# Kernel tuning notes

Hardware: AMD Instinct MI355X
Metric: run time of the kernel (lower is better)

## Reference

```python
import jax, jax.numpy as jnp
import numpy as np

N_NODES = 60000
N_EDGES = 960000
IN_C = 128
HID = 4 * IN_C       # 512
D_CAT = 8 * IN_C     # 1024
D_FC = 16 * IN_C     # 2048
D_L1 = 32 * IN_C     # 4096
OUT_C = 64
BN_EPS = 1e-5
LEAKY_SLOPE = 0.01


def setup_inputs() -> dict:
    key = jax.random.key(0)
    ks = jax.random.split(key, 32)
    d = {}
    d['x'] = jax.random.normal(ks[0], (N_NODES, IN_C), dtype=jnp.float32)
    d['edge_index'] = jax.random.randint(ks[1], (2, N_EDGES), 0, N_NODES, dtype=jnp.int64)

    def lin(k, fan_in, fan_out):
        k1, k2 = jax.random.split(k)
        bound = 1.0 / np.sqrt(fan_in)
        w = jax.random.uniform(k1, (fan_in, fan_out), jnp.float32, -bound, bound)
        b = jax.random.uniform(k2, (fan_out,), jnp.float32, -bound, bound)
        return w, b

    # GIN conv A MLP: Linear(IN_C,HID) -> BN(HID) -> ReLU -> Linear(HID,HID) -> ReLU
    d['w1a'], d['b1a'] = lin(ks[2], IN_C, HID)
    d['gamma_a'] = jnp.ones((HID,), jnp.float32)
    d['beta_a'] = jnp.zeros((HID,), jnp.float32)
    d['mean_a'] = jax.random.normal(ks[3], (HID,), jnp.float32) * 0.1
    d['var_a'] = jax.random.uniform(ks[4], (HID,), jnp.float32, 0.5, 1.5)
    d['w2a'], d['b2a'] = lin(ks[5], HID, HID)
    # GIN conv B MLP
    d['w1b'], d['b1b'] = lin(ks[6], IN_C, HID)
    d['gamma_b'] = jnp.ones((HID,), jnp.float32)
    d['beta_b'] = jnp.zeros((HID,), jnp.float32)
    d['mean_b'] = jax.random.normal(ks[7], (HID,), jnp.float32) * 0.1
    d['var_b'] = jax.random.uniform(ks[8], (HID,), jnp.float32, 0.5, 1.5)
    d['w2b'], d['b2b'] = lin(ks[9], HID, HID)
    # dense head
    d['fc_w'], d['fc_b'] = lin(ks[10], D_CAT, D_FC)
    d['l1_w'], d['l1_b'] = lin(ks[11], D_FC, D_L1)
    d['l2_w'], d['l2_b'] = lin(ks[12], D_L1, D_FC)
    d['out_w'], d['out_b'] = lin(ks[13], D_FC, OUT_C)
    return d


def _gin_conv(x, edge_index, w1, b1, gamma, beta, mean, var, w2, b2):
    # GINConv, eps=0: h_i = MLP(x_i + sum_{j->i} x_j)
    src, dst = edge_index[0], edge_index[1]
    agg = jax.ops.segment_sum(x[src], dst, num_segments=x.shape[0])
    h = x + agg
    h = h @ w1 + b1
    # BatchNorm1d in eval mode (running stats)
    h = (h - mean) * jax.lax.rsqrt(var + BN_EPS) * gamma + beta
    h = jax.nn.relu(h)
    h = jax.nn.relu(h @ w2 + b2)
    return h


def reference(x, edge_index, w1a, b1a, gamma_a, beta_a, mean_a, var_a, w2a, b2a,
              w1b, b1b, gamma_b, beta_b, mean_b, var_b, w2b, b2b,
              fc_w, fc_b, l1_w, l1_b, l2_w, l2_b, out_w, out_b):
    x1 = _gin_conv(x, edge_index, w1a, b1a, gamma_a, beta_a, mean_a, var_a, w2a, b2a)
    x2 = _gin_conv(x, edge_index, w1b, b1b, gamma_b, beta_b, mean_b, var_b, w2b, b2b)
    h = jnp.concatenate([x1, x2], axis=1)               # [N, 8*in]
    h = jax.nn.leaky_relu(h @ fc_w + fc_b, LEAKY_SLOPE)  # dropout is identity in eval
    h = h @ l1_w + l1_b
    h = h @ l2_w + l2_b
    h = jax.nn.sigmoid(h @ out_w + out_b)
    return h
```

## Files before the change

### kernel.cpp

```cpp
#include <hip/hip_runtime.h>


#define NN 60000
#define NE 960000
#define C_IN 128
#define HID 512
#define DCAT 1024
#define DFC 2048
#define DL1 4096
#define OUTC 64

typedef __bf16 bf16x8 __attribute__((ext_vector_type(8)));
typedef float floatx4 __attribute__((ext_vector_type(4)));

__device__ __forceinline__ unsigned short f2b(float f) {
  unsigned int u = __float_as_uint(f);
  unsigned int r = (u + 0x7fffu + ((u >> 16) & 1u)) >> 16;
  return (unsigned short)r;
}

#define GLOAD_LDS16(g, l)                                                     \
  __builtin_amdgcn_global_load_lds(                                           \
      (__attribute__((address_space(1))) void*)(g),                           \
      (__attribute__((address_space(3))) void*)(l), 16, 0, 0)

__global__ void k_bnparams(const float* __restrict__ g,
                           const float* __restrict__ be,
                           const float* __restrict__ mn,
                           const float* __restrict__ vr,
                           const float* __restrict__ b1,
                           float* __restrict__ scale, float* __restrict__ shift) {
  int i = blockIdx.x * 256 + threadIdx.x;
  if (i < HID) {
    float s = g[i] * rsqrtf(vr[i] + 1e-5f);
    scale[i] = s;
    shift[i] = (b1[i] - mn[i]) * s + be[i];
  }
}

__global__ void k_transpose(const float* __restrict__ in,
                            unsigned short* __restrict__ out, int K, int N) {
  __shared__ float t[32][33];
  int n0 = blockIdx.x * 32, k0 = blockIdx.y * 32;
  int tx = threadIdx.x & 31, ty = threadIdx.x >> 5;
#pragma unroll
  for (int i = 0; i < 32; i += 8)
    t[ty + i][tx] = in[(size_t)(k0 + ty + i) * N + n0 + tx];
  __syncthreads();
#pragma unroll
  for (int i = 0; i < 32; i += 8)
    out[(size_t)(n0 + ty + i) * K + k0 + tx] = f2b(t[tx][ty + i]);
}

__global__ void k_deg(const int* __restrict__ dst, int* __restrict__ deg) {
  int e = blockIdx.x * 256 + threadIdx.x;
  if (e < NE) atomicAdd(&deg[dst[e]], 1);
}

__global__ void k_scan1(const int* __restrict__ deg, int* __restrict__ offs,
                        int* __restrict__ bsum) {
  __shared__ int t[256];
  int i = blockIdx.x * 256 + threadIdx.x;
  int v = (i < NN) ? deg[i] : 0;
  t[threadIdx.x] = v;
  __syncthreads();
#pragma unroll
  for (int d = 1; d < 256; d <<= 1) {
    int add = (threadIdx.x >= d) ? t[threadIdx.x - d] : 0;
    __syncthreads();
    t[threadIdx.x] += add;
    __syncthreads();
  }
  if (i < NN) offs[i] = t[threadIdx.x] - v;
  if (threadIdx.x == 255) bsum[blockIdx.x] = t[255];
}

__global__ void k_scan2(int* __restrict__ bsum, int nb) {
  __shared__ int t[256];
  int v = (threadIdx.x < nb) ? bsum[threadIdx.x] : 0;
  t[threadIdx.x] = v;
  __syncthreads();
#pragma unroll
  for (int d = 1; d < 256; d <<= 1) {
    int add = (threadIdx.x >= d) ? t[threadIdx.x - d] : 0;
    __syncthreads();
    t[threadIdx.x] += add;
    __syncthreads();
  }
  if (threadIdx.x < nb) bsum[threadIdx.x] = t[threadIdx.x] - v;
}

__global__ void k_scan3(int* __restrict__ offs, const int* __restrict__ bsum,
                        int* __restrict__ cursor) {
  int i = blockIdx.x * 256 + threadIdx.x;
  if (i < NN) {
    int o = offs[i] + bsum[blockIdx.x];
    offs[i] = o;
    cursor[i] = o;
  }
  if (i == 0) offs[NN] = NE;
}

__global__ void k_bucket(const int* __restrict__ src, const int* __restrict__ dst,
                         int* __restrict__ cursor, int* __restrict__ esrc) {
  int e = blockIdx.x * 256 + threadIdx.x;
  if (e < NE) {
    int slot = atomicAdd(&cursor[dst[e]], 1);
    esrc[slot] = src[e];
  }
}

__global__ void k_agg(const float2* __restrict__ x2, const int* __restrict__ offs,
                      const int* __restrict__ esrc, unsigned int* __restrict__ h0u) {
  int node = blockIdx.x * 4 + (threadIdx.x >> 6);
  if (node >= NN) return;
  int lane = threadIdx.x & 63;
  int beg = offs[node], end = offs[node + 1];
  float2 acc = x2[(size_t)node * 64 + lane];
  for (int j = beg; j < end; j++) {
    int s = esrc[j];
    float2 v = x2[(size_t)s * 64 + lane];
    acc.x += v.x;
    acc.y += v.y;
  }
  h0u[(size_t)node * 64 + lane] =
      (unsigned)f2b(acc.x) | ((unsigned)f2b(acc.y) << 16);
}

template <int EPI>
__device__ __forceinline__ void gemm_epilogue(
    floatx4 (&acc)[8][4], unsigned short* C, const float* bias,
    const float* scale, const float* shift, int M, int N, int ldc, int m0,
    int n0, int w, int quad, int r16) {
#pragma unroll
  for (int j = 0; j < 4; j++) {
    int gn = n0 + w * 64 + j * 16 + r16;
    int cn = gn < N ? gn : 0;
    float p0, p1 = 0.f;
    if constexpr (EPI == 2) {
      p0 = scale[cn];
      p1 = shift[cn];
    } else {
      p0 = bias[cn];
    }
#pragma unroll
    for (int i = 0; i < 8; i++) {
#pragma unroll
      for (int t = 0; t < 4; t++) {
        int gm = m0 + i * 16 + quad * 4 + t;
        if (gm < M && gn < N) {
          float v = acc[i][j][t];
          if constexpr (EPI == 0) {
            v += p0;
            C[(size_t)gm * ldc + gn] = f2b(v);
          } else if constexpr (EPI == 1) {
            v += p0; v = v > 0.f ? v : 0.f;
            C[(size_t)gm * ldc + gn] = f2b(v);
          } else if constexpr (EPI == 2) {
            v = v * p0 + p1; v = v > 0.f ? v : 0.f;
            C[(size_t)gm * ldc + gn] = f2b(v);
          } else if constexpr (EPI == 3) {
            v += p0; v = v > 0.f ? v : 0.01f * v;
            C[(size_t)gm * ldc + gn] = f2b(v);
          } else {
            v += p0;
            v = 1.f / (1.f + __expf(-v));
            ((float*)C)[(size_t)gm * ldc + gn] = v;
          }
        }
      }
    }
  }
}

__device__ __forceinline__ void gemm_swizzle(int M, int N, int& m0, int& n0) {
  const int mt_total = (M + 127) >> 7, nt_total = (N + 255) >> 8;
  int mt, nt;
  if ((nt_total & 7) == 0) {
    const int ntpx = nt_total >> 3;
    const int x = blockIdx.x & 7;
    const int s = blockIdx.x >> 3;
    nt = x * ntpx + (s % ntpx);
    mt = s / ntpx;
  } else {
    const int GM = 8;
    const int full = (mt_total / GM) * GM;
    const int boundary = full * nt_total;
    int id = blockIdx.x;
    if (id < boundary) {
      int per_group = GM * nt_total;
      int g = id / per_group, r = id % per_group;
      mt = g * GM + r % GM;
      nt = r / GM;
    } else {
      int r = id - boundary, gm = mt_total - full;
      mt = full + r % gm;
      nt = r / gm;
    }
  }
  m0 = mt << 7;
  n0 = nt << 8;
}

__device__ __forceinline__ void gemm_swizzle256(int M, int N, int& m0, int& n0) {
  const int mt_total = (M + 255) >> 8, nt_total = N >> 8;
  int mt, nt;
  if ((nt_total & 7) == 0) {
    const int ntpx = nt_total >> 3;
    const int x = blockIdx.x & 7;
    const int s = blockIdx.x >> 3;
    nt = x * ntpx + (s % ntpx);
    mt = s / ntpx;
  } else {
    const int GM = 8;
    const int full = (mt_total / GM) * GM;
    const int boundary = full * nt_total;
    int id = blockIdx.x;
    if (id < boundary) {
      int per_group = GM * nt_total;
      int g = id / per_group, r = id % per_group;
      mt = g * GM + r % GM;
      nt = r / GM;
    } else {
      int r = id - boundary, gm = mt_total - full;
      mt = full + r % gm;
      nt = r / gm;
    }
  }
  m0 = mt << 8;
  n0 = nt << 8;
}

template <int EPI>
__global__ __launch_bounds__(256, 2) void k_gemm_g(
    const unsigned short* __restrict__ A, const unsigned short* __restrict__ Bt,
    unsigned short* __restrict__ C, const float* __restrict__ bias,
    const float* __restrict__ scale, const float* __restrict__ shift,
    int M, int N, int K, int lda, int ldc) {
  __shared__ __align__(16) unsigned short lsA[4][4][128][8];

  const int tid = threadIdx.x;
  const int w = tid >> 6;
  const int lane = tid & 63;
  const int quad = lane >> 4;
  const int r16 = lane & 15;

  int m0, n0;
  gemm_swizzle(M, N, m0, n0);

  const int ra0 = min(m0 + lane, M - 1);
  const int ra1 = min(m0 + 64 + lane, M - 1);
  const unsigned short* pA0 = A + (size_t)ra0 * lda + w * 8;
  const unsigned short* pA1 = A + (size_t)ra1 * lda + w * 8;
  const unsigned short* pB[4];
#pragma unroll
  for (int j = 0; j < 4; j++) {
    int rb = min(n0 + w * 64 + j * 16 + r16, N - 1);
    pB[j] = Bt + (size_t)rb * K + quad * 8;
  }

  floatx4 acc[8][4];
#pragma unroll
  for (int i = 0; i < 8; i++)
#pragma unroll
    for (int j = 0; j < 4; j++) acc[i][j] = (floatx4){0.f, 0.f, 0.f, 0.f};

  const int niter = K >> 5;

#define ISSUE_A(st)                                                           \
  do {                                                                        \
    GLOAD_LDS16(pA0, &lsA[st][w][0][0]);                                      \
    GLOAD_LDS16(pA1, &lsA[st][w][64][0]);                                     \
    pA0 += 32; pA1 += 32;                                                     \
  } while (0)

  ISSUE_A(0);
  if (niter > 1) ISSUE_A(1);
  if (niter > 2) ISSUE_A(2);
  bf16x8 bcur[4], bnxt[4];
#pragma unroll
  for (int j = 0; j < 4; j++) {
    bcur[j] = *(const bf16x8*)pB[j];
    pB[j] += 32;
  }

  int st = 0;
  for (int t = 0; t < niter; t++) {
    if (t + 2 < niter) {
      asm volatile("s_waitcnt vmcnt(8)\n\ts_barrier" ::: "memory");
    } else if (t + 1 < niter) {
      asm volatile("s_waitcnt vmcnt(6)\n\ts_barrier" ::: "memory");
    } else {
      asm volatile("s_waitcnt vmcnt(4)\n\ts_barrier" ::: "memory");
    }
    if (t + 3 < niter) {
      int s3 = st + 3;
      if (s3 >= 4) s3 -= 4;
      ISSUE_A(s3);
    }
    if (t + 1 < niter) {
#pragma unroll
      for (int j = 0; j < 4; j++) {
        bnxt[j] = *(const bf16x8*)pB[j];
        pB[j] += 32;
      }
    }

    bf16x8 af[8];
#pragma unroll
    for (int i = 0; i < 8; i++)
      af[i] = *(const bf16x8*)&lsA[st][quad][i * 16 + r16][0];
#pragma unroll
    for (int j = 0; j < 4; j++)
#pragma unroll
      for (int i = 0; i < 8; i++)
        acc[i][j] = __builtin_amdgcn_mfma_f32_16x16x32_bf16(af[i], bcur[j],
                                                            acc[i][j], 0, 0, 0);
#pragma unroll
    for (int j = 0; j < 4; j++) bcur[j] = bnxt[j];
    st = (st + 1) & 3;
  }
#undef ISSUE_A

  gemm_epilogue<EPI>(acc, C, bias, scale, shift, M, N, ldc, m0, n0, w, quad, r16);
}

template <int EPI>
__global__ __launch_bounds__(512, 2) void k_gemm8(
    const unsigned short* __restrict__ A, const unsigned short* __restrict__ Bt,
    unsigned short* __restrict__ C, const float* __restrict__ bias,
    const float* __restrict__ scale, const float* __restrict__ shift,
    int M, int N, int K, int lda, int ldc) {
  __shared__ __align__(16) unsigned short smem[2][2][256][64];

  const int tid = threadIdx.x;
  const int w = tid >> 6;
  const int lane = tid & 63;
  const int wm = w >> 2;
  const int wn = w & 3;
  const int quad = lane >> 4;
  const int r16 = lane & 15;

  int m0, n0;
  gemm_swizzle256(M, N, m0, n0);

  const int w8l = w * 8 + (lane >> 3);
  const int csrc = (lane & 7) ^ ((lane >> 3) & 7);
  unsigned offA[2][2], offB[2][2];
#pragma unroll
  for (int h = 0; h < 2; h++)
#pragma unroll
    for (int q = 0; q < 2; q++) {
      int ra = m0 + h * 128 + q * 64 + w8l;
      ra = ra < M ? ra : (M - 1);
      offA[h][q] = (unsigned)ra * (unsigned)(lda * 2) + (unsigned)(csrc * 16);
      int rb = n0 + h * 128 + q * 64 + w8l;
      offB[h][q] = (unsigned)rb * (unsigned)(K * 2) + (unsigned)(csrc * 16);
    }
  const char* Ac = (const char*)A;
  const char* Bc = (const char*)Bt;
  char* smc = (char*)smem;
  const unsigned wdst = (unsigned)(w * 1024);

#define STG_A(T_, h_)                                                          \
  do {                                                                         \
    unsigned kb_ = (unsigned)(T_) * 128u;                                      \
    unsigned db_ = (unsigned)(((T_) & 1) << 16) + (unsigned)((h_) * 16384) + wdst; \
    GLOAD_LDS16(Ac + offA[h_][0] + kb_, smc + db_);                            \
    GLOAD_LDS16(Ac + offA[h_][1] + kb_, smc + db_ + 8192u);                    \
  } while (0)
#define STG_B(T_, h_)                                                          \
  do {                                                                         \
    unsigned kb_ = (unsigned)(T_) * 128u;                                      \
    unsigned db_ = (unsigned)(((T_) & 1) << 16) + 32768u +                     \
                   (unsigned)((h_) * 16384) + wdst;                            \
    GLOAD_LDS16(Bc + offB[h_][0] + kb_, smc + db_);                            \
    GLOAD_LDS16(Bc + offB[h_][1] + kb_, smc + db_ + 8192u);                    \
  } while (0)

  const int swz = r16 & 7;
  const unsigned cK0 = (unsigned)(((quad) ^ swz) * 16);
  const unsigned cK1 = (unsigned)(((4 + quad) ^ swz) * 16);
  const unsigned rdA = (unsigned)((wm * 128 + r16) * 128);
  const unsigned rdB = 32768u + (unsigned)((wn * 64 + r16) * 128);

#define RD_A(bo_, i_, c_) (*(const bf16x8*)(smc + (bo_) + rdA + (unsigned)((i_)*2048) + (c_)))
#define RD_B(bo_, j_, c_) (*(const bf16x8*)(smc + (bo_) + rdB + (unsigned)((j_)*2048) + (c_)))

  floatx4 acc[8][4];
#pragma unroll
  for (int i = 0; i < 8; i++)
#pragma unroll
    for (int j = 0; j < 4; j++) acc[i][j] = (floatx4){0.f, 0.f, 0.f, 0.f};

  const int NT = K >> 6;

  STG_B(0, 0); STG_B(0, 1); STG_A(0, 0); STG_A(0, 1);
  if (NT > 1) {
    STG_B(1, 0); STG_B(1, 1); STG_A(1, 0); STG_A(1, 1);
    asm volatile("s_waitcnt vmcnt(8)\n\ts_barrier" ::: "memory");
  } else {
    asm volatile("s_waitcnt vmcnt(0)\n\ts_barrier" ::: "memory");
  }

  bf16x8 aF[4][2], bL[2][2], bH[2][2];

  for (int T = 0; T < NT; T++) {
    const unsigned bo = (unsigned)((T & 1) << 16);
#pragma unroll
    for (int i = 0; i < 4; i++) { aF[i][0] = RD_A(bo, i, cK0); aF[i][1] = RD_A(bo, i, cK1); }
#pragma unroll
    for (int j = 0; j < 2; j++) { bL[j][0] = RD_B(bo, j, cK0); bL[j][1] = RD_B(bo, j, cK1); }
    asm volatile("s_barrier" ::: "memory");
    asm volatile("s_waitcnt lgkmcnt(0)" ::: "memory");
    __builtin_amdgcn_s_setprio(1);
#pragma unroll
    for (int j = 0; j < 2; j++)
#pragma unroll
      for (int i = 0; i < 4; i++) {
        acc[i][j] = __builtin_amdgcn_mfma_f32_16x16x32_bf16(aF[i][0], bL[j][0], acc[i][j], 0, 0, 0);
        acc[i][j] = __builtin_amdgcn_mfma_f32_16x16x32_bf16(aF[i][1], bL[j][1], acc[i][j], 0, 0, 0);
      }
    __builtin_amdgcn_s_setprio(0);
    asm volatile("s_barrier" ::: "memory");
#pragma unroll
    for (int j = 0; j < 2; j++) { bH[j][0] = RD_B(bo, j + 2, cK0); bH[j][1] = RD_B(bo, j + 2, cK1); }
    asm volatile("s_barrier" ::: "memory");
    asm volatile("s_waitcnt lgkmcnt(0)" ::: "memory");
    __builtin_amdgcn_s_setprio(1);
#pragma unroll
    for (int j = 0; j < 2; j++)
#pragma unroll
      for (int i = 0; i < 4; i++) {
        acc[i][j + 2] = __builtin_amdgcn_mfma_f32_16x16x32_bf16(aF[i][0], bH[j][0], acc[i][j + 2], 0, 0, 0);
        acc[i][j + 2] = __builtin_amdgcn_mfma_f32_16x16x32_bf16(aF[i][1], bH[j][1], acc[i][j + 2], 0, 0, 0);
      }
    __builtin_amdgcn_s_setprio(0);
    asm volatile("s_barrier" ::: "memory");
#pragma unroll
    for (int i = 0; i < 4; i++) { aF[i][0] = RD_A(bo, i + 4, cK0); aF[i][1] = RD_A(bo, i + 4, cK1); }
    if (T + 2 < NT) { STG_B(T + 2, 0); STG_B(T + 2, 1); }
    asm volatile("s_barrier" ::: "memory");
    asm volatile("s_waitcnt lgkmcnt(0)" ::: "memory");
    __builtin_amdgcn_s_setprio(1);
#pragma unroll
    for (int j = 0; j < 2; j++)
#pragma unroll
      for (int i = 0; i < 4; i++) {
        acc[i + 4][j + 2] = __builtin_amdgcn_mfma_f32_16x16x32_bf16(aF[i][0], bH[j][0], acc[i + 4][j + 2], 0, 0, 0);
        acc[i + 4][j + 2] = __builtin_amdgcn_mfma_f32_16x16x32_bf16(aF[i][1], bH[j][1], acc[i + 4][j + 2], 0, 0, 0);
      }
    __builtin_amdgcn_s_setprio(0);
    asm volatile("s_barrier" ::: "memory");
    if (T + 2 < NT) { STG_A(T + 2, 0); STG_A(T + 2, 1); }
    asm volatile("s_barrier" ::: "memory");
    __builtin_amdgcn_s_setprio(1);
#pragma unroll
    for (int j = 0; j < 2; j++)
#pragma unroll
      for (int i = 0; i < 4; i++) {
        acc[i + 4][j] = __builtin_amdgcn_mfma_f32_16x16x32_bf16(aF[i][0], bL[j][0], acc[i + 4][j], 0, 0, 0);
        acc[i + 4][j] = __builtin_amdgcn_mfma_f32_16x16x32_bf16(aF[i][1], bL[j][1], acc[i + 4][j], 0, 0, 0);
      }
    __builtin_amdgcn_s_setprio(0);
    if (T + 1 < NT) {
      if (T + 2 < NT) {
        asm volatile("s_waitcnt vmcnt(8)\n\ts_barrier" ::: "memory");
      } else {
        asm volatile("s_waitcnt vmcnt(0)\n\ts_barrier" ::: "memory");
      }
    }
  }
#undef STG_A
#undef STG_B
#undef RD_A
#undef RD_B

  __syncthreads();
  char* eb = smc + (unsigned)(w * 16384);
#pragma unroll
  for (int j = 0; j < 4; j++) {
    int gn = n0 + wn * 64 + j * 16 + r16;
    float p0 = 0.f, p1 = 0.f;
    if constexpr (EPI == 2) {
      p0 = scale[gn];
      p1 = shift[gn];
    } else {
      p0 = bias[gn];
    }
#pragma unroll
    for (int i = 0; i < 8; i++)
#pragma unroll
      for (int t = 0; t < 4; t++) {
        float v = acc[i][j][t];
        if constexpr (EPI == 0) {
          v += p0;
        } else if constexpr (EPI == 1) {
          v += p0; v = v > 0.f ? v : 0.f;
        } else if constexpr (EPI == 2) {
          v = v * p0 + p1; v = v > 0.f ? v : 0.f;
        } else {
          v += p0; v = v > 0.f ? v : 0.01f * v;
        }
        int row = i * 16 + quad * 4 + t;
        int col = j * 16 + r16;
        *(unsigned short*)(eb + row * 128 + (((col >> 3) ^ (row & 7)) << 4) +
                           ((col & 7) << 1)) = f2b(v);
      }
  }
#pragma unroll
  for (int r8 = 0; r8 < 16; r8++) {
    int row = r8 * 8 + (lane >> 3);
    int chunkG = lane & 7;
    bf16x8 vv = *(const bf16x8*)(eb + row * 128 + ((chunkG ^ (lane >> 3)) << 4));
    int gm = m0 + wm * 128 + row;
    if (gm < M)
      *(bf16x8*)(C + (size_t)gm * ldc + (n0 + wn * 64 + chunkG * 8)) = vv;
  }
}

extern "C" void kernel_launch(void* const* d_in, const int* in_sizes, int n_in,
                              void* d_out, int out_size, void* d_ws,
                              size_t ws_size, hipStream_t stream) {
  typedef const float* cf;
  cf x = (cf)d_in[0];
  const int* ei = (const int*)d_in[1];
  const int* srcI = ei;
  const int* dstI = ei + NE;
  cf w1a = (cf)d_in[2],  b1a = (cf)d_in[3];
  cf ga = (cf)d_in[4],   bea = (cf)d_in[5];
  cf mna = (cf)d_in[6],  vra = (cf)d_in[7];
  cf w2a = (cf)d_in[8],  b2a = (cf)d_in[9];
  cf w1b = (cf)d_in[10], b1b = (cf)d_in[11];
  cf gb = (cf)d_in[12],  beb = (cf)d_in[13];
  cf mnb = (cf)d_in[14], vrb = (cf)d_in[15];
  cf w2b = (cf)d_in[16], b2b = (cf)d_in[17];
  cf fc_w = (cf)d_in[18], fc_b = (cf)d_in[19];
  cf l1_w = (cf)d_in[20], l1_b = (cf)d_in[21];
  cf l2_w = (cf)d_in[22], l2_b = (cf)d_in[23];
  cf ow = (cf)d_in[24],   ob = (cf)d_in[25];
  float* outf = (float*)d_out;

  char* ws = (char*)d_ws;
  size_t off = 0;
  auto carve = [&](size_t bytes) {
    void* p = ws + off;
    off += (bytes + 255) & ~(size_t)255;
    return p;
  };
  unsigned short* wt1ab = (unsigned short*)carve((size_t)DCAT * C_IN * 2);
  unsigned short* wt2a = (unsigned short*)carve((size_t)HID * HID * 2);
  unsigned short* wt2b = (unsigned short*)carve((size_t)HID * HID * 2);
  unsigned short* wtfc = (unsigned short*)carve((size_t)DFC * DCAT * 2);
  unsigned short* wtl1 = (unsigned short*)carve((size_t)DL1 * DFC * 2);
  unsigned short* wtl2 = (unsigned short*)carve((size_t)DFC * DL1 * 2);
  unsigned short* wtout = (unsigned short*)carve((size_t)OUTC * DFC * 2);
  float* scale_ab = (float*)carve(DCAT * 4);
  float* shift_ab = (float*)carve(DCAT * 4);
  unsigned short* h0 = (unsigned short*)carve((size_t)NN * C_IN * 2);

  size_t off_overlay = off;
  int* deg = (int*)carve((size_t)NN * 4);
  int* offs = (int*)carve((size_t)(NN + 1) * 4);
  int* cursor = (int*)carve((size_t)NN * 4);
  int* bsum = (int*)carve(256 * 4);
  int* esrc = (int*)carve((size_t)NE * 4);

  off = off_overlay;
  size_t rem = (ws_size > off + 4096) ? (ws_size - off - 4096) : 0;
  int mchunk = (int)(rem / ((DFC + DL1) * 2));
  if (mchunk > 15104) mchunk = 15104;
  mchunk &= ~127;
  if (mchunk < 128) mchunk = 128;
  unsigned short* bufA = (unsigned short*)carve((size_t)mchunk * DFC * 2);
  unsigned short* bufB = (unsigned short*)carve((size_t)mchunk * DL1 * 2);
  (void)in_sizes; (void)n_in; (void)out_size;

  k_bnparams<<<2, 256, 0, stream>>>(ga, bea, mna, vra, b1a, scale_ab, shift_ab);
  k_bnparams<<<2, 256, 0, stream>>>(gb, beb, mnb, vrb, b1b, scale_ab + HID,
                                    shift_ab + HID);
  k_transpose<<<dim3(HID / 32, C_IN / 32), 256, 0, stream>>>(w1a, wt1ab, C_IN, HID);
  k_transpose<<<dim3(HID / 32, C_IN / 32), 256, 0, stream>>>(
      w1b, wt1ab + (size_t)HID * C_IN, C_IN, HID);
  k_transpose<<<dim3(HID / 32, HID / 32), 256, 0, stream>>>(w2a, wt2a, HID, HID);
  k_transpose<<<dim3(HID / 32, HID / 32), 256, 0, stream>>>(w2b, wt2b, HID, HID);
  k_transpose<<<dim3(DFC / 32, DCAT / 32), 256, 0, stream>>>(fc_w, wtfc, DCAT, DFC);
  k_transpose<<<dim3(DL1 / 32, DFC / 32), 256, 0, stream>>>(l1_w, wtl1, DFC, DL1);
  k_transpose<<<dim3(DFC / 32, DL1 / 32), 256, 0, stream>>>(l2_w, wtl2, DL1, DFC);
  k_transpose<<<dim3(OUTC / 32, DFC / 32), 256, 0, stream>>>(ow, wtout, DFC, OUTC);

  const int NB_NODE = (NN + 255) / 256;
  hipMemsetAsync(deg, 0, (size_t)NN * 4, stream);
  k_deg<<<(NE + 255) / 256, 256, 0, stream>>>(dstI, deg);
  k_scan1<<<NB_NODE, 256, 0, stream>>>(deg, offs, bsum);
  k_scan2<<<1, 256, 0, stream>>>(bsum, NB_NODE);
  k_scan3<<<NB_NODE, 256, 0, stream>>>(offs, bsum, cursor);
  k_bucket<<<(NE + 255) / 256, 256, 0, stream>>>(srcI, dstI, cursor, esrc);
  k_agg<<<(NN + 3) / 4, 256, 0, stream>>>((const float2*)x, offs, esrc,
                                          (unsigned int*)h0);

  auto gemm = [&](int var, int epi, const unsigned short* A,
                  const unsigned short* Bt, unsigned short* Cp, cf bias,
                  const float* sc, const float* sh, int M, int N, int K,
                  int lda, int ldc) {
    if (var == 2) {
      dim3 g(((M + 255) / 256) * (N / 256));
      switch (epi) {
        case 0: k_gemm8<0><<<g, 512, 0, stream>>>(A, Bt, Cp, bias, sc, sh, M, N, K, lda, ldc); break;
        default: k_gemm8<3><<<g, 512, 0, stream>>>(A, Bt, Cp, bias, sc, sh, M, N, K, lda, ldc); break;
      }
    } else {
      dim3 g(((M + 127) / 128) * ((N + 255) / 256));
      switch (epi) {
        case 0: k_gemm_g<0><<<g, 256, 0, stream>>>(A, Bt, Cp, bias, sc, sh, M, N, K, lda, ldc); break;
        case 1: k_gemm_g<1><<<g, 256, 0, stream>>>(A, Bt, Cp, bias, sc, sh, M, N, K, lda, ldc); break;
        case 2: k_gemm_g<2><<<g, 256, 0, stream>>>(A, Bt, Cp, bias, sc, sh, M, N, K, lda, ldc); break;
        case 3: k_gemm_g<3><<<g, 256, 0, stream>>>(A, Bt, Cp, bias, sc, sh, M, N, K, lda, ldc); break;
        default: k_gemm_g<4><<<g, 256, 0, stream>>>(A, Bt, Cp, bias, sc, sh, M, N, K, lda, ldc); break;
      }
    }
  };

  for (int m0 = 0; m0 < NN; m0 += mchunk) {
    const int M = (NN - m0 < mchunk) ? (NN - m0) : mchunk;
    const unsigned short* h0c = h0 + (size_t)m0 * C_IN;
    unsigned short* outc = (unsigned short*)(outf + (size_t)m0 * OUTC);
    gemm(1, 2, h0c, wt1ab, bufA, nullptr, scale_ab, shift_ab, M, DCAT, C_IN, C_IN, DCAT);
    gemm(1, 1, bufA, wt2a, bufB, b2a, nullptr, nullptr, M, HID, HID, DCAT, DCAT);
    gemm(1, 1, bufA + HID, wt2b, bufB + HID, b2b, nullptr, nullptr, M, HID, HID, DCAT, DCAT);
    gemm(2, 3, bufB, wtfc, bufA, fc_b, nullptr, nullptr, M, DFC, DCAT, DCAT, DFC);
    gemm(2, 0, bufA, wtl1, bufB, l1_b, nullptr, nullptr, M, DL1, DFC, DFC, DL1);
    gemm(2, 0, bufB, wtl2, bufA, l2_b, nullptr, nullptr, M, DFC, DL1, DL1, DFC);
    gemm(1, 4, bufA, wtout, outc, ob, nullptr, nullptr, M, OUTC, DFC, DFC, OUTC);
  }
}
```

Baseline: 3.279 ms.

## Load B fragments directly from global into registers, triple-buffer A in LDS

The 256x256 GEMM kernel stops staging the B (weight) tile through LDS. Each wave now loads its B fragments straight from global memory into registers one tile ahead. Only A goes through LDS, now with three buffers and a single barrier per K-tile instead of several. The aim is to cut LDS traffic, LDS footprint and barrier count so loads and MFMAs overlap better. In exchange, B reads from global are uncoalesced 16-byte fragments repeated across waves, raising L2 traffic and register pressure. The epilogue is split into two halves to fit the smaller LDS.

Result: slower. 5.003 ms (+52.6%).

```diff
diff --git a/kernel.cpp b/kernel.cpp
--- a/kernel.cpp
+++ b/kernel.cpp
@@ -331,7 +331,7 @@
     unsigned short* __restrict__ C, const float* __restrict__ bias,
     const float* __restrict__ scale, const float* __restrict__ shift,
     int M, int N, int K, int lda, int ldc) {
-  __shared__ __align__(16) unsigned short smem[2][2][256][64];
+  __shared__ __align__(16) unsigned short smem[3][256][64];
 
   const int tid = threadIdx.x;
   const int w = tid >> 6;
@@ -346,7 +346,7 @@
 
   const int w8l = w * 8 + (lane >> 3);
   const int csrc = (lane & 7) ^ ((lane >> 3) & 7);
-  unsigned offA[2][2], offB[2][2];
+  unsigned offA[2][2];
 #pragma unroll
   for (int h = 0; h < 2; h++)
 #pragma unroll
@@ -354,38 +354,35 @@
       int ra = m0 + h * 128 + q * 64 + w8l;
       ra = ra < M ? ra : (M - 1);
       offA[h][q] = (unsigned)ra * (unsigned)(lda * 2) + (unsigned)(csrc * 16);
-      int rb = n0 + h * 128 + q * 64 + w8l;
-      offB[h][q] = (unsigned)rb * (unsigned)(K * 2) + (unsigned)(csrc * 16);
     }
   const char* Ac = (const char*)A;
-  const char* Bc = (const char*)Bt;
   char* smc = (char*)smem;
   const unsigned wdst = (unsigned)(w * 1024);
 
-#define STG_A(T_, h_)                                                          \
-  do {                                                                         \
-    unsigned kb_ = (unsigned)(T_) * 128u;                                      \
-    unsigned db_ = (unsigned)(((T_) & 1) << 16) + (unsigned)((h_) * 16384) + wdst; \
-    GLOAD_LDS16(Ac + offA[h_][0] + kb_, smc + db_);                            \
-    GLOAD_LDS16(Ac + offA[h_][1] + kb_, smc + db_ + 8192u);                    \
+#define STG_A2(T_)                                                            \
+  do {                                                                        \
+    unsigned kb_ = (unsigned)(T_) * 128u;                                     \
+    unsigned db_ = (unsigned)(((T_) % 3) * 32768) + wdst;                     \
+    GLOAD_LDS16(Ac + offA[0][0] + kb_, smc + db_);                            \
+    GLOAD_LDS16(Ac + offA[0][1] + kb_, smc + db_ + 8192u);                    \
+    GLOAD_LDS16(Ac + offA[1][0] + kb_, smc + db_ + 16384u);                   \
+    GLOAD_LDS16(Ac + offA[1][1] + kb_, smc + db_ + 24576u);                   \
   } while (0)
-#define STG_B(T_, h_)                                                          \
-  do {                                                                         \
-    unsigned kb_ = (unsigned)(T_) * 128u;                                      \
-    unsigned db_ = (unsigned)(((T_) & 1) << 16) + 32768u +                     \
-                   (unsigned)((h_) * 16384) + wdst;                            \
-    GLOAD_LDS16(Bc + offB[h_][0] + kb_, smc + db_);                            \
-    GLOAD_LDS16(Bc + offB[h_][1] + kb_, smc + db_ + 8192u);                    \
-  } while (0)
+
+  const unsigned short* pB[4];
+#pragma unroll
+  for (int j = 0; j < 4; j++) {
+    int rb = n0 + wn * 64 + j * 16 + r16;
+    pB[j] = Bt + (size_t)rb * K + quad * 8;
+  }
+#define LD_B(j_, ks_, t_) (*(const bf16x8*)(pB[j_] + (t_)*64 + (ks_)*32))
 
   const int swz = r16 & 7;
   const unsigned cK0 = (unsigned)(((quad) ^ swz) * 16);
   const unsigned cK1 = (unsigned)(((4 + quad) ^ swz) * 16);
   const unsigned rdA = (unsigned)((wm * 128 + r16) * 128);
-  const unsigned rdB = 32768u + (unsigned)((wn * 64 + r16) * 128);
 
 #define RD_A(bo_, i_, c_) (*(const bf16x8*)(smc + (bo_) + rdA + (unsigned)((i_)*2048) + (c_)))
-#define RD_B(bo_, j_, c_) (*(const bf16x8*)(smc + (bo_) + rdB + (unsigned)((j_)*2048) + (c_)))
 
   floatx4 acc[8][4];
 #pragma unroll
@@ -395,127 +392,132 @@
 
   const int NT = K >> 6;
 
-  STG_B(0, 0); STG_B(0, 1); STG_A(0, 0); STG_A(0, 1);
+#define MM2(i0_, AF, BF)                                                      \
+  do {                                                                        \
+    __builtin_amdgcn_s_setprio(1);                                            \
+    _Pragma("unroll")                                                         \
+    for (int jj = 0; jj < 4; jj++) {                                          \
+      acc[(i0_)][jj] = __builtin_amdgcn_mfma_f32_16x16x32_bf16(               \
+          AF[0][0], BF[jj][0], acc[(i0_)][jj], 0, 0, 0);                      \
+      acc[(i0_)][jj] = __builtin_amdgcn_mfma_f32_16x16x32_bf16(               \
+          AF[0][1], BF[jj][1], acc[(i0_)][jj], 0, 0, 0);                      \
+      acc[(i0_) + 1][jj] = __builtin_amdgcn_mfma_f32_16x16x32_bf16(           \
+          AF[1][0], BF[jj][0], acc[(i0_) + 1][jj], 0, 0, 0);                  \
+      acc[(i0_) + 1][jj] = __builtin_amdgcn_mfma_f32_16x16x32_bf16(           \
+          AF[1][1], BF[jj][1], acc[(i0_) + 1][jj], 0, 0, 0);                  \
+    }                                                                         \
+    __builtin_amdgcn_s_setprio(0);                                            \
+  } while (0)
+
+  bf16x8 aP[2][2], aQ[2][2];
+  bf16x8 bA[4][2], bB[4][2];
+
+#define TILE(T_, BC, BN)                                                      \
+  do {                                                                        \
+    const unsigned bb = (unsigned)(((T_) % 3) * 32768);                       \
+                       \
+    aQ[0][0] = RD_A(bb, 2, cK0); aQ[0][1] = RD_A(bb, 2, cK1);                 \
+    aQ[1][0] = RD_A(bb, 3, cK0); aQ[1][1] = RD_A(bb, 3, cK1);                 \
+    if ((T_) + 2 < NT) STG_A2((T_) + 2);                                      \
+    MM2(0, aP, BC);                                                           \
+                         \
+    aP[0][0] = RD_A(bb, 4, cK0); aP[0][1] = RD_A(bb, 4, cK1);                 \
+    aP[1][0] = RD_A(bb, 5, cK0); aP[1][1] = RD_A(bb, 5, cK1);                 \
+    MM2(2, aQ, BC);                                                           \
+    if ((T_) + 1 < NT) {                                                      \
+      BN[0][0] = LD_B(0, 0, (T_) + 1); BN[0][1] = LD_B(0, 1, (T_) + 1);       \
+      BN[1][0] = LD_B(1, 0, (T_) + 1); BN[1][1] = LD_B(1, 1, (T_) + 1);       \
+    }                                                                         \
+                         \
+    aQ[0][0] = RD_A(bb, 6, cK0); aQ[0][1] = RD_A(bb, 6, cK1);                 \
+    aQ[1][0] = RD_A(bb, 7, cK0); aQ[1][1] = RD_A(bb, 7, cK1);                 \
+    MM2(4, aP, BC);                                                           \
+    if ((T_) + 1 < NT) {                                                      \
+      BN[2][0] = LD_B(2, 0, (T_) + 1); BN[2][1] = LD_B(2, 1, (T_) + 1);       \
+      BN[3][0] = LD_B(3, 0, (T_) + 1); BN[3][1] = LD_B(3, 1, (T_) + 1);       \
+    }                                                                         \
+        \
+    if ((T_) + 1 < NT) {                                                      \
+      if ((T_) + 2 < NT) {                                                    \
+        asm volatile("s_waitcnt vmcnt(12)\n\ts_barrier" ::: "memory");        \
+      } else {                                                                \
+        asm volatile("s_waitcnt vmcnt(8)\n\ts_barrier" ::: "memory");         \
+      }                                                                       \
+      const unsigned nb = (unsigned)((((T_) + 1) % 3) * 32768);               \
+      aP[0][0] = RD_A(nb, 0, cK0); aP[0][1] = RD_A(nb, 0, cK1);               \
+      aP[1][0] = RD_A(nb, 1, cK0); aP[1][1] = RD_A(nb, 1, cK1);               \
+    }                                                                         \
+    MM2(6, aQ, BC);                                                           \
+  } while (0)
+
+  STG_A2(0);
+  if (NT > 1) STG_A2(1);
+#pragma unroll
+  for (int j = 0; j < 4; j++) {
+    bA[j][0] = LD_B(j, 0, 0);
+    bA[j][1] = LD_B(j, 1, 0);
+  }
   if (NT > 1) {
-    STG_B(1, 0); STG_B(1, 1); STG_A(1, 0); STG_A(1, 1);
+    asm volatile("s_waitcnt vmcnt(12)\n\ts_barrier" ::: "memory");
+  } else {
     asm volatile("s_waitcnt vmcnt(8)\n\ts_barrier" ::: "memory");
-  } else {
-    asm volatile("s_waitcnt vmcnt(0)\n\ts_barrier" ::: "memory");
-  }
-
-  bf16x8 aF[4][2], bL[2][2], bH[2][2];
-
-  for (int T = 0; T < NT; T++) {
-    const unsigned bo = (unsigned)((T & 1) << 16);
-#pragma unroll
-    for (int i = 0; i < 4; i++) { aF[i][0] = RD_A(bo, i, cK0); aF[i][1] = RD_A(bo, i, cK1); }
-#pragma unroll
-    for (int j = 0; j < 2; j++) { bL[j][0] = RD_B(bo, j, cK0); bL[j][1] = RD_B(bo, j, cK1); }
-    asm volatile("s_barrier" ::: "memory");
-    asm volatile("s_waitcnt lgkmcnt(0)" ::: "memory");
-    __builtin_amdgcn_s_setprio(1);
-#pragma unroll
-    for (int j = 0; j < 2; j++)
-#pragma unroll
-      for (int i = 0; i < 4; i++) {
-        acc[i][j] = __builtin_amdgcn_mfma_f32_16x16x32_bf16(aF[i][0], bL[j][0], acc[i][j], 0, 0, 0);
-        acc[i][j] = __builtin_amdgcn_mfma_f32_16x16x32_bf16(aF[i][1], bL[j][1], acc[i][j], 0, 0, 0);
+  }
+  aP[0][0] = RD_A(0u, 0, cK0); aP[0][1] = RD_A(0u, 0, cK1);
+  aP[1][0] = RD_A(0u, 1, cK0); aP[1][1] = RD_A(0u, 1, cK1);
+
+  for (int T = 0; T < NT; T += 2) {
+    TILE(T, bA, bB);
+    TILE(T + 1, bB, bA);
+  }
+#undef TILE
+#undef MM2
+#undef STG_A2
+#undef RD_A
+#undef LD_B
+
+  __syncthreads();
+  char* eb = smc + (unsigned)(w * 8192);
+#pragma unroll
+  for (int p = 0; p < 2; p++) {
+#pragma unroll
+    for (int j = 0; j < 4; j++) {
+      int gn = n0 + wn * 64 + j * 16 + r16;
+      float p0 = 0.f, p1 = 0.f;
+      if constexpr (EPI == 2) {
+        p0 = scale[gn];
+        p1 = shift[gn];
+      } else {
+        p0 = bias[gn];
       }
-    __builtin_amdgcn_s_setprio(0);
-    asm volatile("s_barrier" ::: "memory");
-#pragma unroll
-    for (int j = 0; j < 2; j++) { bH[j][0] = RD_B(bo, j + 2, cK0); bH[j][1] = RD_B(bo, j + 2, cK1); }
-    asm volatile("s_barrier" ::: "memory");
-    asm volatile("s_waitcnt lgkmcnt(0)" ::: "memory");
-    __builtin_amdgcn_s_setprio(1);
-#pragma unroll
-    for (int j = 0; j < 2; j++)
-#pragma unroll
-      for (int i = 0; i < 4; i++) {
-        acc[i][j + 2] = __builtin_amdgcn_mfma_f32_16x16x32_bf16(aF[i][0], bH[j][0], acc[i][j + 2], 0, 0, 0);
-        acc[i][j + 2] = __builtin_amdgcn_mfma_f32_16x16x32_bf16(aF[i][1], bH[j][1], acc[i][j + 2], 0, 0, 0);
-      }
-    __builtin_amdgcn_s_setprio(0);
-    asm volatile("s_barrier" ::: "memory");
-#pragma unroll
-    for (int i = 0; i < 4; i++) { aF[i][0] = RD_A(bo, i + 4, cK0); aF[i][1] = RD_A(bo, i + 4, cK1); }
-    if (T + 2 < NT) { STG_B(T + 2, 0); STG_B(T + 2, 1); }
-    asm volatile("s_barrier" ::: "memory");
-    asm volatile("s_waitcnt lgkmcnt(0)" ::: "memory");
-    __builtin_amdgcn_s_setprio(1);
-#pragma unroll
-    for (int j = 0; j < 2; j++)
-#pragma unroll
-      for (int i = 0; i < 4; i++) {
-        acc[i + 4][j + 2] = __builtin_amdgcn_mfma_f32_16x16x32_bf16(aF[i][0], bH[j][0], acc[i + 4][j + 2], 0, 0, 0);
-        acc[i + 4][j + 2] = __builtin_amdgcn_mfma_f32_16x16x32_bf16(aF[i][1], bH[j][1], acc[i + 4][j + 2], 0, 0, 0);
-      }
-    __builtin_amdgcn_s_setprio(0);
-    asm volatile("s_barrier" ::: "memory");
-    if (T + 2 < NT) { STG_A(T + 2, 0); STG_A(T + 2, 1); }
-    asm volatile("s_barrier" ::: "memory");
-    __builtin_amdgcn_s_setprio(1);
-#pragma unroll
-    for (int j = 0; j < 2; j++)
-#pragma unroll
-      for (int i = 0; i < 4; i++) {
-        acc[i + 4][j] = __builtin_amdgcn_mfma_f32_16x16x32_bf16(aF[i][0], bL[j][0], acc[i + 4][j], 0, 0, 0);
-        acc[i + 4][j] = __builtin_amdgcn_mfma_f32_16x16x32_bf16(aF[i][1], bL[j][1], acc[i + 4][j], 0, 0, 0);
-      }
-    __builtin_amdgcn_s_setprio(0);
-    if (T + 1 < NT) {
-      if (T + 2 < NT) {
-        asm volatile("s_waitcnt vmcnt(8)\n\ts_barrier" ::: "memory");
-      } else {
-        asm volatile("s_waitcnt vmcnt(0)\n\ts_barrier" ::: "memory");
-      }
-    }
-  }
-#undef STG_A
-#undef STG_B
-#undef RD_A
-#undef RD_B
-
-  __syncthreads();
-  char* eb = smc + (unsigned)(w * 16384);
-#pragma unroll
-  for (int j = 0; j < 4; j++) {
-    int gn = n0 + wn * 64 + j * 16 + r16;
-    float p0 = 0.f, p1 = 0.f;
-    if constexpr (EPI == 2) {
-      p0 = scale[gn];
-      p1 = shift[gn];
-    } else {
-      p0 = bias[gn];
-    }
-#pragma unroll
-    for (int i = 0; i < 8; i++)
-#pragma unroll
-      for (int t = 0; t < 4; t++) {
-        float v = acc[i][j][t];
-        if constexpr (EPI == 0) {
-          v += p0;
-        } else if constexpr (EPI == 1) {
-          v += p0; v = v > 0.f ? v : 0.f;
-        } else if constexpr (EPI == 2) {
-          v = v * p0 + p1; v = v > 0.f ? v : 0.f;
-        } else {
-          v += p0; v = v > 0.f ? v : 0.01f * v;
+#pragma unroll
+      for (int i = 0; i < 4; i++)
+#pragma unroll
+        for (int t = 0; t < 4; t++) {
+          float v = acc[p * 4 + i][j][t];
+          if constexpr (EPI == 0) {
+            v += p0;
+          } else if constexpr (EPI == 1) {
+            v += p0; v = v > 0.f ? v : 0.f;
+          } else if constexpr (EPI == 2) {
+            v = v * p0 + p1; v = v > 0.f ? v : 0.f;
+          } else {
+            v += p0; v = v > 0.f ? v : 0.01f * v;
+          }
+          int row = i * 16 + quad * 4 + t;
+          int col = j * 16 + r16;
+          *(unsigned short*)(eb + row * 128 + (((col >> 3) ^ (row & 7)) << 4) +
+                             ((col & 7) << 1)) = f2b(v);
         }
-        int row = i * 16 + quad * 4 + t;
-        int col = j * 16 + r16;
-        *(unsigned short*)(eb + row * 128 + (((col >> 3) ^ (row & 7)) << 4) +
-                           ((col & 7) << 1)) = f2b(v);
-      }
-  }
-#pragma unroll
-  for (int r8 = 0; r8 < 16; r8++) {
-    int row = r8 * 8 + (lane >> 3);
-    int chunkG = lane & 7;
-    bf16x8 vv = *(const bf16x8*)(eb + row * 128 + ((chunkG ^ (lane >> 3)) << 4));
-    int gm = m0 + wm * 128 + row;
-    if (gm < M)
-      *(bf16x8*)(C + (size_t)gm * ldc + (n0 + wn * 64 + chunkG * 8)) = vv;
+    }
+#pragma unroll
+    for (int r8 = 0; r8 < 8; r8++) {
+      int row = r8 * 8 + (lane >> 3);
+      int chunkG = lane & 7;
+      bf16x8 vv = *(const bf16x8*)(eb + row * 128 + ((chunkG ^ (lane >> 3)) << 4));
+      int gm = m0 + wm * 128 + p * 64 + row;
+      if (gm < M)
+        *(bf16x8*)(C + (size_t)gm * ldc + (n0 + wn * 64 + chunkG * 8)) = vv;
+    }
   }
 }
 
```

## Restructure GEMM main loop to single-stage prefetch with register-pipelined A fragments

Applied to the files above, without the earlier changes.

The GEMM K-loop drops the two-tile-deep global→LDS prefetch and its barrier-separated ping-pong phases. It now prefetches only the next tile into the other LDS buffer. Inside the loop it loads all B fragments once, then double-buffers A fragments in registers (aP/aQ) so LDS reads overlap the MFMA groups, with no intra-iteration barriers. This cuts barrier and sync overhead, but each iteration now waits for all outstanding global loads (vmcnt(0)), which may expose more memory latency than the deeper prefetch did.

Measured after the change: 3.151 ms. -3.9%, faster.

```diff
diff --git a/kernel.cpp b/kernel.cpp
--- a/kernel.cpp
+++ b/kernel.cpp
@@ -395,82 +395,50 @@
 
   const int NT = K >> 6;
 
-  STG_B(0, 0); STG_B(0, 1); STG_A(0, 0); STG_A(0, 1);
-  if (NT > 1) {
-    STG_B(1, 0); STG_B(1, 1); STG_A(1, 0); STG_A(1, 1);
-    asm volatile("s_waitcnt vmcnt(8)\n\ts_barrier" ::: "memory");
-  } else {
-    asm volatile("s_waitcnt vmcnt(0)\n\ts_barrier" ::: "memory");
-  }
-
-  bf16x8 aF[4][2], bL[2][2], bH[2][2];
+#define MM2(i0_, AF)                                                          \
+  do {                                                                        \
+    __builtin_amdgcn_s_setprio(1);                                            \
+    _Pragma("unroll")                                                         \
+    for (int jj = 0; jj < 4; jj++) {                                          \
+      acc[(i0_)][jj] = __builtin_amdgcn_mfma_f32_16x16x32_bf16(               \
+          AF[0][0], bF[jj][0], acc[(i0_)][jj], 0, 0, 0);                      \
+      acc[(i0_)][jj] = __builtin_amdgcn_mfma_f32_16x16x32_bf16(               \
+          AF[0][1], bF[jj][1], acc[(i0_)][jj], 0, 0, 0);                      \
+      acc[(i0_) + 1][jj] = __builtin_amdgcn_mfma_f32_16x16x32_bf16(           \
+          AF[1][0], bF[jj][0], acc[(i0_) + 1][jj], 0, 0, 0);                  \
+      acc[(i0_) + 1][jj] = __builtin_amdgcn_mfma_f32_16x16x32_bf16(           \
+          AF[1][1], bF[jj][1], acc[(i0_) + 1][jj], 0, 0, 0);                  \
+    }                                                                         \
+    __builtin_amdgcn_s_setprio(0);                                            \
+  } while (0)
+
+  STG_A(0, 0); STG_A(0, 1); STG_B(0, 0); STG_B(0, 1);
+  asm volatile("s_waitcnt vmcnt(0)\n\ts_barrier" ::: "memory");
+
+  bf16x8 bF[4][2], aP[2][2], aQ[2][2];
 
   for (int T = 0; T < NT; T++) {
     const unsigned bo = (unsigned)((T & 1) << 16);
 #pragma unroll
-    for (int i = 0; i < 4; i++) { aF[i][0] = RD_A(bo, i, cK0); aF[i][1] = RD_A(bo, i, cK1); }
-#pragma unroll
-    for (int j = 0; j < 2; j++) { bL[j][0] = RD_B(bo, j, cK0); bL[j][1] = RD_B(bo, j, cK1); }
-    asm volatile("s_barrier" ::: "memory");
-    asm volatile("s_waitcnt lgkmcnt(0)" ::: "memory");
-    __builtin_amdgcn_s_setprio(1);
-#pragma unroll
-    for (int j = 0; j < 2; j++)
-#pragma unroll
-      for (int i = 0; i < 4; i++) {
-        acc[i][j] = __builtin_amdgcn_mfma_f32_16x16x32_bf16(aF[i][0], bL[j][0], acc[i][j], 0, 0, 0);
-        acc[i][j] = __builtin_amdgcn_mfma_f32_16x16x32_bf16(aF[i][1], bL[j][1], acc[i][j], 0, 0, 0);
-      }
-    __builtin_amdgcn_s_setprio(0);
-    asm volatile("s_barrier" ::: "memory");
-#pragma unroll
-    for (int j = 0; j < 2; j++) { bH[j][0] = RD_B(bo, j + 2, cK0); bH[j][1] = RD_B(bo, j + 2, cK1); }
-    asm volatile("s_barrier" ::: "memory");
-    asm volatile("s_waitcnt lgkmcnt(0)" ::: "memory");
-    __builtin_amdgcn_s_setprio(1);
-#pragma unroll
-    for (int j = 0; j < 2; j++)
-#pragma unroll
-      for (int i = 0; i < 4; i++) {
-        acc[i][j + 2] = __builtin_amdgcn_mfma_f32_16x16x32_bf16(aF[i][0], bH[j][0], acc[i][j + 2], 0, 0, 0);
-        acc[i][j + 2] = __builtin_amdgcn_mfma_f32_16x16x32_bf16(aF[i][1], bH[j][1], acc[i][j + 2], 0, 0, 0);
-      }
-    __builtin_amdgcn_s_setprio(0);
-    asm volatile("s_barrier" ::: "memory");
-#pragma unroll
-    for (int i = 0; i < 4; i++) { aF[i][0] = RD_A(bo, i + 4, cK0); aF[i][1] = RD_A(bo, i + 4, cK1); }
-    if (T + 2 < NT) { STG_B(T + 2, 0); STG_B(T + 2, 1); }
-    asm volatile("s_barrier" ::: "memory");
-    asm volatile("s_waitcnt lgkmcnt(0)" ::: "memory");
-    __builtin_amdgcn_s_setprio(1);
-#pragma unroll
-    for (int j = 0; j < 2; j++)
-#pragma unroll
-      for (int i = 0; i < 4; i++) {
-        acc[i + 4][j + 2] = __builtin_amdgcn_mfma_f32_16x16x32_bf16(aF[i][0], bH[j][0], acc[i + 4][j + 2], 0, 0, 0);
-        acc[i + 4][j + 2] = __builtin_amdgcn_mfma_f32_16x16x32_bf16(aF[i][1], bH[j][1], acc[i + 4][j + 2], 0, 0, 0);
-      }
-    __builtin_amdgcn_s_setprio(0);
-    asm volatile("s_barrier" ::: "memory");
-    if (T + 2 < NT) { STG_A(T + 2, 0); STG_A(T + 2, 1); }
-    asm volatile("s_barrier" ::: "memory");
-    __builtin_amdgcn_s_setprio(1);
-#pragma unroll
-    for (int j = 0; j < 2; j++)
-#pragma unroll
-      for (int i = 0; i < 4; i++) {
-        acc[i + 4][j] = __builtin_amdgcn_mfma_f32_16x16x32_bf16(aF[i][0], bL[j][0], acc[i + 4][j], 0, 0, 0);
-        acc[i + 4][j] = __builtin_amdgcn_mfma_f32_16x16x32_bf16(aF[i][1], bL[j][1], acc[i + 4][j], 0, 0, 0);
-      }
-    __builtin_amdgcn_s_setprio(0);
+    for (int j = 0; j < 4; j++) { bF[j][0] = RD_B(bo, j, cK0); bF[j][1] = RD_B(bo, j, cK1); }
+    aP[0][0] = RD_A(bo, 0, cK0); aP[0][1] = RD_A(bo, 0, cK1);
+    aP[1][0] = RD_A(bo, 1, cK0); aP[1][1] = RD_A(bo, 1, cK1);
+    if (T + 1 < NT) { STG_A(T + 1, 0); STG_A(T + 1, 1); STG_B(T + 1, 0); STG_B(T + 1, 1); }
+    aQ[0][0] = RD_A(bo, 2, cK0); aQ[0][1] = RD_A(bo, 2, cK1);
+    aQ[1][0] = RD_A(bo, 3, cK0); aQ[1][1] = RD_A(bo, 3, cK1);
+    MM2(0, aP);
+    aP[0][0] = RD_A(bo, 4, cK0); aP[0][1] = RD_A(bo, 4, cK1);
+    aP[1][0] = RD_A(bo, 5, cK0); aP[1][1] = RD_A(bo, 5, cK1);
+    MM2(2, aQ);
+    aQ[0][0] = RD_A(bo, 6, cK0); aQ[0][1] = RD_A(bo, 6, cK1);
+    aQ[1][0] = RD_A(bo, 7, cK0); aQ[1][1] = RD_A(bo, 7, cK1);
+    MM2(4, aP);
+    MM2(6, aQ);
     if (T + 1 < NT) {
-      if (T + 2 < NT) {
-        asm volatile("s_waitcnt vmcnt(8)\n\ts_barrier" ::: "memory");
-      } else {
-        asm volatile("s_waitcnt vmcnt(0)\n\ts_barrier" ::: "memory");
-      }
-    }
-  }
+      asm volatile("s_waitcnt vmcnt(0)\n\ts_barrier" ::: "memory");
+    }
+  }
+#undef MM2
 #undef STG_A
 #undef STG_B
 #undef RD_A
```
